# Kernel optimization log

Hardware: AMD Instinct MI355X
Metric: run time of the kernel (lower is better)

## Reference

```python
import jax, jax.numpy as jnp
import numpy as np

# ---- model hyperparameters (match init_kwargs) ----
THRESHOLD = 1.0
DECAY = 0.9
RESET = 0.0
BATCH = 256
INPUT_DIM = 1024
HIDDEN_DIM = 2048
OUTPUT_DIM = 10
NUM_LAYERS = 2
SIM_STEPS = 100
SPIKE_PROB = 0.2  # density of input spike bins


def setup_inputs() -> dict:
    key = jax.random.key(0)
    k1, k2, k3, k4 = jax.random.split(key, 4)
    # binary spike bins: [B, input_dim, T]
    input_bins = (jax.random.uniform(k1, (BATCH, INPUT_DIM, SIM_STEPS)) < SPIKE_PROB).astype(jnp.float32)
    W_ih = jax.random.normal(k2, (INPUT_DIM, HIDDEN_DIM), dtype=jnp.float32) * 0.1
    W_hh = jax.random.normal(k3, (NUM_LAYERS - 1, HIDDEN_DIM, HIDDEN_DIM), dtype=jnp.float32) * 0.1
    W_ho = jax.random.normal(k4, (HIDDEN_DIM, OUTPUT_DIM), dtype=jnp.float32) * 0.1
    return {"input_bins": input_bins, "W_ih": W_ih, "W_hh": W_hh, "W_ho": W_ho}


def _lif_step(v, current):
    """One leaky-integrate-and-fire update. v, current: [B, N]."""
    v = v * DECAY + current
    spiked = v >= THRESHOLD
    spikes = jnp.where(spiked, 1.0, 0.0).astype(v.dtype)
    v = jnp.where(spiked, RESET, v)
    return v, spikes


def reference(input_bins, W_ih, W_hh, W_ho):
    B = input_bins.shape[0]
    T = input_bins.shape[2]
    x = jnp.transpose(input_bins, (2, 0, 1))  # [T, B, input_dim]
    v_hidden = tuple(jnp.zeros((B, W_ih.shape[1]), input_bins.dtype) for _ in range(NUM_LAYERS))
    v_out = jnp.zeros((B, W_ho.shape[1]), input_bins.dtype)

    def step(carry, inp_t):
        vs, vo = carry
        vs = list(vs)
        vs[0], s = _lif_step(vs[0], inp_t @ W_ih)
        for i in range(NUM_LAYERS - 1):
            vs[i + 1], s = _lif_step(vs[i + 1], s @ W_hh[i])
        # modulator signal is 0 here -> output_input * (1 + 0*0.1) = output_input
        vo, s_out = _lif_step(vo, s @ W_ho)
        return (tuple(vs), vo), s_out

    _, out_spikes = jax.lax.scan(step, (v_hidden, v_out), x)  # [T, B, output_dim]
    output_rates = out_spikes.sum(axis=0) / T  # [B, output_dim]
    return output_rates
```

## Files before the change

### kernel.cpp

```cpp
#include <hip/hip_runtime.h>
#include <hip/hip_bf16.h>


#define B 256
#define IN_DIM 1024
#define HID 2048
#define OUT_DIM 10
#define T_STEPS 100
#define NCH 4
#define RT (T_STEPS * B)

typedef unsigned long long ull;
typedef int v4i __attribute__((ext_vector_type(4)));

template<int K>
__global__ __launch_bounds__(256) void cvt_w_i8(
    const float* __restrict__ W, signed char* __restrict__ Bq)
{
    constexpr int WPR = K / 64;
    size_t id = (size_t)blockIdx.x * 256 + threadIdx.x;
    if (id >= (size_t)(K / 4) * HID) return;
    int n  = (int)(id % HID);
    int kg = (int)(id / HID);
    int k0 = kg * 4;
    signed char dig[4][4];
#pragma unroll
    for (int i = 0; i < 4; ++i) {
        double w = (double)W[(size_t)(k0 + i) * HID + n];
        long long V = __double2ll_rn(w * 2147483648.0);
#pragma unroll
        for (int c = 0; c < 3; ++c) {
            int r = (int)(signed char)(V & 0xFF);
            dig[c][i] = (signed char)r;
            V = (V - r) >> 8;
        }
        dig[3][i] = (signed char)V;
    }
    int wb = k0 >> 6, lk = (k0 >> 4) & 3, jj = k0 & 15;
    int nb32 = n >> 5, ct = (n >> 4) & 1, li = n & 15;
    int lane = lk * 16 + li;
    size_t base = ((size_t)nb32 * WPR + wb) * 8192 + (size_t)lane * 16 + jj;
#pragma unroll
    for (int c = 0; c < 4; ++c) {
        int pc = (c < 3) ? (c * 2 + ct) : (6 + ct);
        unsigned pk = (unsigned)(unsigned char)dig[c][0]
                    | ((unsigned)(unsigned char)dig[c][1] << 8)
                    | ((unsigned)(unsigned char)dig[c][2] << 16)
                    | ((unsigned)(unsigned char)dig[c][3] << 24);
        *reinterpret_cast<unsigned*>(Bq + base + (size_t)pc * 1024) = pk;
    }
}

__global__ __launch_bounds__(256) void cvt_who(
    const float* __restrict__ who, double* __restrict__ Who64)
{
    int i = blockIdx.x * 256 + threadIdx.x;
    if (i < HID * OUT_DIM) Who64[i] = (double)who[i];
}

__global__ __launch_bounds__(256) void bitpack_input(
    const float* __restrict__ inp, ull* __restrict__ XbitsT)
{
    int g = blockIdx.x * 4 + (threadIdx.x >> 6);
    int lane = threadIdx.x & 63;
    int b = g >> 4;
    int ig = g & 15;
    int i = ig * 64 + lane;
    const float4* p = (const float4*)(inp + ((size_t)b * IN_DIM + i) * T_STEPS);
    ull* dst = XbitsT + (size_t)ig * RT + b;
#pragma unroll 1
    for (int t4 = 0; t4 < T_STEPS / 4; ++t4) {
        float4 v = p[t4];
        ull m0 = __ballot(v.x > 0.5f);
        ull m1 = __ballot(v.y > 0.5f);
        ull m2 = __ballot(v.z > 0.5f);
        ull m3 = __ballot(v.w > 0.5f);
        if (lane == 0) {
            dst[(size_t)(t4 * 4 + 0) * B] = m0;
            dst[(size_t)(t4 * 4 + 1) * B] = m1;
            dst[(size_t)(t4 * 4 + 2) * B] = m2;
            dst[(size_t)(t4 * 4 + 3) * B] = m3;
        }
    }
}

template<int K>
__global__ __launch_bounds__(256, 3) void gemm_i8(
    const ull* __restrict__ bitsT, int row_base,
    const signed char* __restrict__ Bq, float* __restrict__ C)
{
    constexpr int WPR = K / 64;
    constexpr int NP  = WPR / 2;
    __shared__ __align__(16) signed char blds[6][8192];

    const int tid = threadIdx.x;
    const int lane = tid & 63;
    const int wv = __builtin_amdgcn_readfirstlane(tid >> 6);
    const int row0 = blockIdx.x * 128;
    const int c0 = blockIdx.y * 32;
    const int li = lane & 15;
    const int lk = lane >> 4;
    const int sh = lk * 16;
    const int r0l = wv * 32;

    const signed char* __restrict__ bsrc = Bq + (size_t)blockIdx.y * WPR * 8192;
    const ull* __restrict__ m0p = bitsT + (row_base + row0 + r0l + li);
    const ull* __restrict__ m1p = m0p + 16;

    auto stage_b = [&](int w, int slot) {
        const signed char* src = bsrc + (size_t)w * 8192 + lane * 16;
        signed char* db = &blds[0][0] + slot * 8192;
        __builtin_amdgcn_global_load_lds(
            (const __attribute__((address_space(1))) unsigned int*)(src + wv * 1024),
            (__attribute__((address_space(3))) unsigned int*)(db + wv * 1024), 16, 0, 0);
        __builtin_amdgcn_global_load_lds(
            (const __attribute__((address_space(1))) unsigned int*)(src + (wv + 4) * 1024),
            (__attribute__((address_space(3))) unsigned int*)(db + (wv + 4) * 1024), 16, 0, 0);
    };

    stage_b(0, 0);
    stage_b(1, 1);
    stage_b(2, 2);
    stage_b(3, 3);
    ull r0[4], r1[4];
#pragma unroll
    for (int u = 0; u < 4; ++u) {
        r0[u] = m0p[(size_t)u * RT];
        r1[u] = m1p[(size_t)u * RT];
    }
    __syncthreads();

    v4i acc[2][2][NCH];
#pragma unroll
    for (int g = 0; g < 2; ++g)
#pragma unroll
        for (int t = 0; t < 2; ++t)
#pragma unroll
            for (int c = 0; c < NCH; ++c) acc[g][t][c] = (v4i){0, 0, 0, 0};

    int s0 = 0;
#pragma unroll 1
    for (int p2 = 0; p2 < NP; p2 += 2) {
#pragma unroll
        for (int pp = 0; pp < 2; ++pp) {
            const int w0 = (p2 + pp) * 2;
            const int u0 = w0 & 3, u1 = (w0 + 1) & 3;
            int s1 = s0 + 1; if (s1 >= 6) s1 -= 6;
            int t0 = s0 + 4; if (t0 >= 6) t0 -= 6;
            int t1 = s0 + 5; if (t1 >= 6) t1 -= 6;

            int wn0 = w0 + 4; if (wn0 >= WPR) wn0 -= WPR;
            int wn1 = w0 + 5; if (wn1 >= WPR) wn1 -= WPR;
            stage_b(wn0, t0);
            stage_b(wn1, t1);
            ull m00 = r0[u0], m01 = r1[u0];
            ull m10 = r0[u1], m11 = r1[u1];
            r0[u0] = m0p[(size_t)wn0 * RT];
            r1[u0] = m1p[(size_t)wn0 * RT];
            r0[u1] = m0p[(size_t)wn1 * RT];
            r1[u1] = m1p[(size_t)wn1 * RT];

            {
                unsigned sa = (unsigned)(m00 >> sh) & 0xFFFFu;
                unsigned sb = (unsigned)(m01 >> sh) & 0xFFFFu;
                v4i a0, a1;
#pragma unroll
                for (int d = 0; d < 4; ++d) {
                    a0[d] = (int)((((sa >> (4 * d)) & 0xFu) * 0x00204081u) & 0x01010101u);
                    a1[d] = (int)((((sb >> (4 * d)) & 0xFu) * 0x00204081u) & 0x01010101u);
                }
                const signed char* bb = &blds[0][0] + s0 * 8192 + lane * 16;
                __builtin_amdgcn_s_setprio(1);
#pragma unroll
                for (int c = 0; c < NCH; ++c) {
#pragma unroll
                    for (int t = 0; t < 2; ++t) {
                        v4i b = *(const v4i*)(bb + (c * 2 + t) * 1024);
                        acc[0][t][c] = __builtin_amdgcn_mfma_i32_16x16x64_i8(a0, b, acc[0][t][c], 0, 0, 0);
                        acc[1][t][c] = __builtin_amdgcn_mfma_i32_16x16x64_i8(a1, b, acc[1][t][c], 0, 0, 0);
                    }
                }
                __builtin_amdgcn_s_setprio(0);
            }
            {
                unsigned sa = (unsigned)(m10 >> sh) & 0xFFFFu;
                unsigned sb = (unsigned)(m11 >> sh) & 0xFFFFu;
                v4i a0, a1;
#pragma unroll
                for (int d = 0; d < 4; ++d) {
                    a0[d] = (int)((((sa >> (4 * d)) & 0xFu) * 0x00204081u) & 0x01010101u);
                    a1[d] = (int)((((sb >> (4 * d)) & 0xFu) * 0x00204081u) & 0x01010101u);
                }
                const signed char* bb = &blds[0][0] + s1 * 8192 + lane * 16;
                __builtin_amdgcn_s_setprio(1);
#pragma unroll
                for (int c = 0; c < NCH; ++c) {
#pragma unroll
                    for (int t = 0; t < 2; ++t) {
                        v4i b = *(const v4i*)(bb + (c * 2 + t) * 1024);
                        acc[0][t][c] = __builtin_amdgcn_mfma_i32_16x16x64_i8(a0, b, acc[0][t][c], 0, 0, 0);
                        acc[1][t][c] = __builtin_amdgcn_mfma_i32_16x16x64_i8(a1, b, acc[1][t][c], 0, 0, 0);
                    }
                }
                __builtin_amdgcn_s_setprio(0);
            }

            __asm__ __volatile__("s_waitcnt vmcnt(8)\n\ts_barrier" ::: "memory");
            s0 += 2; if (s0 >= 6) s0 -= 6;
        }
    }

#pragma unroll
    for (int g = 0; g < 2; ++g) {
#pragma unroll
        for (int t = 0; t < 2; ++t) {
#pragma unroll
            for (int r = 0; r < 4; ++r) {
                long long V = (long long)acc[g][t][3][r];
                V = (V << 8) + (long long)acc[g][t][2][r];
                V = (V << 8) + (long long)acc[g][t][1][r];
                V = (V << 8) + (long long)acc[g][t][0][r];
                C[(size_t)(row0 + r0l + g * 16 + lk * 4 + r) * HID + c0 + t * 16 + li] =
                    (float)((double)V * 0x1p-31);
            }
        }
    }
}

__global__ __launch_bounds__(256) void gemm_out(
    const ull* __restrict__ bitsT, int row_base,
    const double* __restrict__ W, double* __restrict__ C3)
{
    __shared__ double part[3][64][OUT_DIM];
    const int lane = threadIdx.x & 63;
    const int sl = threadIdx.x >> 6;
    const int row = blockIdx.x * 64 + lane;

    double acc[OUT_DIM];
#pragma unroll
    for (int j = 0; j < OUT_DIM; ++j) acc[j] = 0.0;

    for (int w = sl * 8; w < sl * 8 + 8; ++w) {
        ull m = bitsT[(size_t)w * RT + row_base + row];
        const double* __restrict__ wk = W + (size_t)(w * 64) * OUT_DIM;
#pragma unroll 4
        for (int kk = 0; kk < 64; ++kk) {
            double bd = (double)(unsigned int)(m & 1ull);
            m >>= 1;
#pragma unroll
            for (int j = 0; j < OUT_DIM; ++j)
                acc[j] = fma(bd, wk[j], acc[j]);
            wk += OUT_DIM;
        }
    }
    if (sl) {
#pragma unroll
        for (int j = 0; j < OUT_DIM; ++j) part[sl - 1][lane][j] = acc[j];
    }
    __syncthreads();
    if (sl == 0) {
        double* __restrict__ crow = C3 + (size_t)row * OUT_DIM;
#pragma unroll
        for (int j = 0; j < OUT_DIM; ++j)
            crow[j] = acc[j] + part[0][lane][j] + part[1][lane][j] + part[2][lane][j];
    }
}

__global__ __launch_bounds__(256) void lif_scan(
    const float* __restrict__ C, double* __restrict__ vstate,
    ull* __restrict__ SbitsT, int row_base, int Tl, int first)
{
    int g = blockIdx.x * 4 + (threadIdx.x >> 6);
    int lane = threadIdx.x & 63;
    int b = g >> 5;
    int ng = g & 31;
    int n = ng * 64 + lane;
    const float* __restrict__ Cp = C + (size_t)b * HID + n;
    ull* __restrict__ Sp = SbitsT + (size_t)ng * RT + row_base + b;
    double v = first ? 0.0 : vstate[(size_t)b * HID + n];
    int tl = 0;
    for (; tl + 4 <= Tl; tl += 4) {
        float c0 = Cp[(size_t)(tl + 0) * (B * HID)];
        float c1 = Cp[(size_t)(tl + 1) * (B * HID)];
        float c2 = Cp[(size_t)(tl + 2) * (B * HID)];
        float c3 = Cp[(size_t)(tl + 3) * (B * HID)];
#pragma unroll
        for (int i = 0; i < 4; ++i) {
            float cc = (i == 0) ? c0 : (i == 1) ? c1 : (i == 2) ? c2 : c3;
            v = v * 0.9 + (double)cc;
            bool s = (v >= 1.0);
            if (s) v = 0.0;
            ull mask = __ballot(s);
            if (lane == 0) Sp[(size_t)(tl + i) * B] = mask;
        }
    }
    for (; tl < Tl; ++tl) {
        double c = (double)Cp[(size_t)tl * (B * HID)];
        v = v * 0.9 + c;
        bool s = (v >= 1.0);
        if (s) v = 0.0;
        ull mask = __ballot(s);
        if (lane == 0) Sp[(size_t)tl * B] = mask;
    }
    vstate[(size_t)b * HID + n] = v;
}

__global__ __launch_bounds__(256) void lif_out(
    const double* __restrict__ C3, double* __restrict__ vstate,
    int* __restrict__ cnt_state, float* __restrict__ out, int Tl, int first)
{
    int tid = blockIdx.x * 256 + threadIdx.x;
    if (tid >= B * OUT_DIM) return;
    int b = tid / OUT_DIM, o = tid % OUT_DIM;
    const double* __restrict__ Cp = C3 + (size_t)b * OUT_DIM + o;
    double v = first ? 0.0 : vstate[tid];
    int cnt = first ? 0 : cnt_state[tid];
    int tl = 0;
    for (; tl + 4 <= Tl; tl += 4) {
        double c0 = Cp[(size_t)(tl + 0) * (B * OUT_DIM)];
        double c1 = Cp[(size_t)(tl + 1) * (B * OUT_DIM)];
        double c2 = Cp[(size_t)(tl + 2) * (B * OUT_DIM)];
        double c3 = Cp[(size_t)(tl + 3) * (B * OUT_DIM)];
#pragma unroll
        for (int i = 0; i < 4; ++i) {
            double cc = (i == 0) ? c0 : (i == 1) ? c1 : (i == 2) ? c2 : c3;
            v = v * 0.9 + cc;
            if (v >= 1.0) { cnt++; v = 0.0; }
        }
    }
    for (; tl < Tl; ++tl) {
        double c = Cp[(size_t)tl * (B * OUT_DIM)];
        v = v * 0.9 + c;
        if (v >= 1.0) { cnt++; v = 0.0; }
    }
    vstate[tid] = v;
    cnt_state[tid] = cnt;
    out[tid] = (float)((double)cnt / (double)T_STEPS);
}

extern "C" void kernel_launch(void* const* d_in, const int* in_sizes, int n_in,
                              void* d_out, int out_size, void* d_ws, size_t ws_size,
                              hipStream_t stream) {
    const float* inp = (const float*)d_in[0];
    const float* wih = (const float*)d_in[1];
    const float* whh = (const float*)d_in[2];
    const float* who = (const float*)d_in[3];
    float* out = (float*)d_out;

    unsigned char* p = (unsigned char*)d_ws;
    auto alloc = [&](size_t sz) -> void* {
        void* r = (void*)p;
        p += (sz + 255) & ~(size_t)255;
        return r;
    };
    signed char* Bq1 = (signed char*)alloc((size_t)NCH * HID * IN_DIM + 4096);
    signed char* Bq2 = (signed char*)alloc((size_t)NCH * HID * HID + 4096);
    double* Who64 = (double*)alloc((size_t)HID * OUT_DIM * 8);
    ull* XbitsT = (ull*)alloc((size_t)16 * RT * 8);
    ull* S1T    = (ull*)alloc((size_t)32 * RT * 8);
    ull* S2T    = (ull*)alloc((size_t)32 * RT * 8);
    double* v1 = (double*)alloc((size_t)B * HID * 8);
    double* v2 = (double*)alloc((size_t)B * HID * 8);
    double* vo = (double*)alloc((size_t)B * OUT_DIM * 8);
    int* cnts  = (int*)alloc((size_t)B * OUT_DIM * 4);

    size_t used = (size_t)(p - (unsigned char*)d_ws);
    size_t remain = (ws_size > used) ? (ws_size - used) : 0;
    size_t per_t = (size_t)B * HID * 4 + (size_t)B * OUT_DIM * 8 + 1024;
    int CH = (int)(remain / per_t);
    if (CH > T_STEPS) CH = T_STEPS;
    if (CH < 1) CH = 1;
    double* C3 = (double*)alloc((size_t)CH * B * OUT_DIM * 8);
    float* C   = (float*)alloc((size_t)CH * B * HID * 4);

    cvt_w_i8<IN_DIM><<<((IN_DIM / 4) * HID + 255) / 256, 256, 0, stream>>>(wih, Bq1);
    cvt_w_i8<HID><<<((HID / 4) * HID + 255) / 256, 256, 0, stream>>>(whh, Bq2);
    cvt_who<<<(HID * OUT_DIM + 255) / 256, 256, 0, stream>>>(who, Who64);
    bitpack_input<<<(B * (IN_DIM / 64)) / 4, 256, 0, stream>>>(inp, XbitsT);

    for (int t0 = 0; t0 < T_STEPS; t0 += CH) {
        int L = T_STEPS - t0;
        if (L > CH) L = CH;
        int rows = L * B;
        int first = (t0 == 0) ? 1 : 0;

        gemm_i8<IN_DIM><<<dim3(rows / 128, HID / 32), 256, 0, stream>>>(
            XbitsT, t0 * B, Bq1, C);
        lif_scan<<<(B * (HID / 64)) / 4, 256, 0, stream>>>(
            C, v1, S1T, t0 * B, L, first);

        gemm_i8<HID><<<dim3(rows / 128, HID / 32), 256, 0, stream>>>(
            S1T, t0 * B, Bq2, C);
        lif_scan<<<(B * (HID / 64)) / 4, 256, 0, stream>>>(
            C, v2, S2T, t0 * B, L, first);

        gemm_out<<<rows / 64, 256, 0, stream>>>(S2T, t0 * B, Who64, C3);
        lif_out<<<(B * OUT_DIM + 255) / 256, 256, 0, stream>>>(
            C3, vo, cnts, out, L, first);
    }
}
```

Baseline: 999.0 us.

## Double the gemm_i8 row tile to 256 rows per block for B reuse

Each wave now computes 64 rows (four 16-row groups) instead of 32, so a block covers 256 rows. Every B fragment read from LDS feeds four MFMAs instead of two, which halves B staging traffic per output and the grid size. The cost is twice the accumulator registers, with occupancy lowered from 3 to 2 blocks per CU, and more outstanding spike-mask loads, so the wait count is raised to 12. The weight packing index change is a cosmetic equivalence, since for c=3 the old and new pc are the same.

```diff
diff --git a/kernel.cpp b/kernel.cpp
--- a/kernel.cpp
+++ b/kernel.cpp
@@ -42,7 +42,7 @@
     size_t base = ((size_t)nb32 * WPR + wb) * 8192 + (size_t)lane * 16 + jj;
 #pragma unroll
     for (int c = 0; c < 4; ++c) {
-        int pc = (c < 3) ? (c * 2 + ct) : (6 + ct);
+        int pc = c * 2 + ct;
         unsigned pk = (unsigned)(unsigned char)dig[c][0]
                     | ((unsigned)(unsigned char)dig[c][1] << 8)
                     | ((unsigned)(unsigned char)dig[c][2] << 16)
@@ -85,7 +85,7 @@
 }
 
 template<int K>
-__global__ __launch_bounds__(256, 3) void gemm_i8(
+__global__ __launch_bounds__(256, 2) void gemm_i8(
     const ull* __restrict__ bitsT, int row_base,
     const signed char* __restrict__ Bq, float* __restrict__ C)
 {
@@ -96,16 +96,15 @@
     const int tid = threadIdx.x;
     const int lane = tid & 63;
     const int wv = __builtin_amdgcn_readfirstlane(tid >> 6);
-    const int row0 = blockIdx.x * 128;
+    const int row0 = blockIdx.x * 256;
     const int c0 = blockIdx.y * 32;
     const int li = lane & 15;
     const int lk = lane >> 4;
     const int sh = lk * 16;
-    const int r0l = wv * 32;
+    const int r0l = wv * 64;
 
     const signed char* __restrict__ bsrc = Bq + (size_t)blockIdx.y * WPR * 8192;
-    const ull* __restrict__ m0p = bitsT + (row_base + row0 + r0l + li);
-    const ull* __restrict__ m1p = m0p + 16;
+    const ull* __restrict__ mp = bitsT + (row_base + row0 + r0l + li);
 
     auto stage_b = [&](int w, int slot) {
         const signed char* src = bsrc + (size_t)w * 8192 + lane * 16;
@@ -122,17 +121,17 @@
     stage_b(1, 1);
     stage_b(2, 2);
     stage_b(3, 3);
-    ull r0[4], r1[4];
-#pragma unroll
-    for (int u = 0; u < 4; ++u) {
-        r0[u] = m0p[(size_t)u * RT];
-        r1[u] = m1p[(size_t)u * RT];
-    }
+    ull r[4][4];
+#pragma unroll
+    for (int u = 0; u < 4; ++u)
+#pragma unroll
+        for (int g = 0; g < 4; ++g)
+            r[u][g] = mp[(size_t)u * RT + g * 16];
     __syncthreads();
 
-    v4i acc[2][2][NCH];
-#pragma unroll
-    for (int g = 0; g < 2; ++g)
+    v4i acc[4][2][NCH];
+#pragma unroll
+    for (int g = 0; g < 4; ++g)
 #pragma unroll
         for (int t = 0; t < 2; ++t)
 #pragma unroll
@@ -146,28 +145,29 @@
             const int w0 = (p2 + pp) * 2;
             const int u0 = w0 & 3, u1 = (w0 + 1) & 3;
             int s1 = s0 + 1; if (s1 >= 6) s1 -= 6;
-            int t0 = s0 + 4; if (t0 >= 6) t0 -= 6;
-            int t1 = s0 + 5; if (t1 >= 6) t1 -= 6;
+            int t0s = s0 + 4; if (t0s >= 6) t0s -= 6;
+            int t1s = s0 + 5; if (t1s >= 6) t1s -= 6;
 
             int wn0 = w0 + 4; if (wn0 >= WPR) wn0 -= WPR;
             int wn1 = w0 + 5; if (wn1 >= WPR) wn1 -= WPR;
-            stage_b(wn0, t0);
-            stage_b(wn1, t1);
-            ull m00 = r0[u0], m01 = r1[u0];
-            ull m10 = r0[u1], m11 = r1[u1];
-            r0[u0] = m0p[(size_t)wn0 * RT];
-            r1[u0] = m1p[(size_t)wn0 * RT];
-            r0[u1] = m0p[(size_t)wn1 * RT];
-            r1[u1] = m1p[(size_t)wn1 * RT];
+            stage_b(wn0, t0s);
+            stage_b(wn1, t1s);
+            ull m0[4], m1[4];
+#pragma unroll
+            for (int g = 0; g < 4; ++g) { m0[g] = r[u0][g]; m1[g] = r[u1][g]; }
+#pragma unroll
+            for (int g = 0; g < 4; ++g) r[u0][g] = mp[(size_t)wn0 * RT + g * 16];
+#pragma unroll
+            for (int g = 0; g < 4; ++g) r[u1][g] = mp[(size_t)wn1 * RT + g * 16];
 
             {
-                unsigned sa = (unsigned)(m00 >> sh) & 0xFFFFu;
-                unsigned sb = (unsigned)(m01 >> sh) & 0xFFFFu;
-                v4i a0, a1;
-#pragma unroll
-                for (int d = 0; d < 4; ++d) {
-                    a0[d] = (int)((((sa >> (4 * d)) & 0xFu) * 0x00204081u) & 0x01010101u);
-                    a1[d] = (int)((((sb >> (4 * d)) & 0xFu) * 0x00204081u) & 0x01010101u);
+                v4i a[4];
+#pragma unroll
+                for (int g = 0; g < 4; ++g) {
+                    unsigned s = (unsigned)(m0[g] >> sh) & 0xFFFFu;
+#pragma unroll
+                    for (int d = 0; d < 4; ++d)
+                        a[g][d] = (int)((((s >> (4 * d)) & 0xFu) * 0x00204081u) & 0x01010101u);
                 }
                 const signed char* bb = &blds[0][0] + s0 * 8192 + lane * 16;
                 __builtin_amdgcn_s_setprio(1);
@@ -176,20 +176,21 @@
 #pragma unroll
                     for (int t = 0; t < 2; ++t) {
                         v4i b = *(const v4i*)(bb + (c * 2 + t) * 1024);
-                        acc[0][t][c] = __builtin_amdgcn_mfma_i32_16x16x64_i8(a0, b, acc[0][t][c], 0, 0, 0);
-                        acc[1][t][c] = __builtin_amdgcn_mfma_i32_16x16x64_i8(a1, b, acc[1][t][c], 0, 0, 0);
+#pragma unroll
+                        for (int g = 0; g < 4; ++g)
+                            acc[g][t][c] = __builtin_amdgcn_mfma_i32_16x16x64_i8(a[g], b, acc[g][t][c], 0, 0, 0);
                     }
                 }
                 __builtin_amdgcn_s_setprio(0);
             }
             {
-                unsigned sa = (unsigned)(m10 >> sh) & 0xFFFFu;
-                unsigned sb = (unsigned)(m11 >> sh) & 0xFFFFu;
-                v4i a0, a1;
-#pragma unroll
-                for (int d = 0; d < 4; ++d) {
-                    a0[d] = (int)((((sa >> (4 * d)) & 0xFu) * 0x00204081u) & 0x01010101u);
-                    a1[d] = (int)((((sb >> (4 * d)) & 0xFu) * 0x00204081u) & 0x01010101u);
+                v4i a[4];
+#pragma unroll
+                for (int g = 0; g < 4; ++g) {
+                    unsigned s = (unsigned)(m1[g] >> sh) & 0xFFFFu;
+#pragma unroll
+                    for (int d = 0; d < 4; ++d)
+                        a[g][d] = (int)((((s >> (4 * d)) & 0xFu) * 0x00204081u) & 0x01010101u);
                 }
                 const signed char* bb = &blds[0][0] + s1 * 8192 + lane * 16;
                 __builtin_amdgcn_s_setprio(1);
@@ -198,29 +199,30 @@
 #pragma unroll
                     for (int t = 0; t < 2; ++t) {
                         v4i b = *(const v4i*)(bb + (c * 2 + t) * 1024);
-                        acc[0][t][c] = __builtin_amdgcn_mfma_i32_16x16x64_i8(a0, b, acc[0][t][c], 0, 0, 0);
-                        acc[1][t][c] = __builtin_amdgcn_mfma_i32_16x16x64_i8(a1, b, acc[1][t][c], 0, 0, 0);
+#pragma unroll
+                        for (int g = 0; g < 4; ++g)
+                            acc[g][t][c] = __builtin_amdgcn_mfma_i32_16x16x64_i8(a[g], b, acc[g][t][c], 0, 0, 0);
                     }
                 }
                 __builtin_amdgcn_s_setprio(0);
             }
 
-            __asm__ __volatile__("s_waitcnt vmcnt(8)\n\ts_barrier" ::: "memory");
+            __asm__ __volatile__("s_waitcnt vmcnt(12)\n\ts_barrier" ::: "memory");
             s0 += 2; if (s0 >= 6) s0 -= 6;
         }
     }
 
 #pragma unroll
-    for (int g = 0; g < 2; ++g) {
+    for (int g = 0; g < 4; ++g) {
 #pragma unroll
         for (int t = 0; t < 2; ++t) {
 #pragma unroll
-            for (int r = 0; r < 4; ++r) {
-                long long V = (long long)acc[g][t][3][r];
-                V = (V << 8) + (long long)acc[g][t][2][r];
-                V = (V << 8) + (long long)acc[g][t][1][r];
-                V = (V << 8) + (long long)acc[g][t][0][r];
-                C[(size_t)(row0 + r0l + g * 16 + lk * 4 + r) * HID + c0 + t * 16 + li] =
+            for (int rr = 0; rr < 4; ++rr) {
+                long long V = (long long)acc[g][t][3][rr];
+                V = (V << 8) + (long long)acc[g][t][2][rr];
+                V = (V << 8) + (long long)acc[g][t][1][rr];
+                V = (V << 8) + (long long)acc[g][t][0][rr];
+                C[(size_t)(row0 + r0l + g * 16 + lk * 4 + rr) * HID + c0 + t * 16 + li] =
                     (float)((double)V * 0x1p-31);
             }
         }
@@ -384,12 +386,12 @@
         int rows = L * B;
         int first = (t0 == 0) ? 1 : 0;
 
-        gemm_i8<IN_DIM><<<dim3(rows / 128, HID / 32), 256, 0, stream>>>(
+        gemm_i8<IN_DIM><<<dim3(rows / 256, HID / 32), 256, 0, stream>>>(
             XbitsT, t0 * B, Bq1, C);
         lif_scan<<<(B * (HID / 64)) / 4, 256, 0, stream>>>(
             C, v1, S1T, t0 * B, L, first);
 
-        gemm_i8<HID><<<dim3(rows / 128, HID / 32), 256, 0, stream>>>(
+        gemm_i8<HID><<<dim3(rows / 256, HID / 32), 256, 0, stream>>>(
             S1T, t0 * B, Bq2, C);
         lif_scan<<<(B * (HID / 64)) / 4, 256, 0, stream>>>(
             C, v2, S2T, t0 * B, L, first);
```

Result: slower. 1.021 ms (+2.2%).

## Software-pipeline spike-mask expansion into MFMA loop with scheduling barriers

Applied to the files above, without the earlier changes.

Expands the A-operand spike bit masks for the next k-step while the current step's int8 MFMAs run, using double-buffered fragment registers and sched_group_barrier to interleave MFMA, LDS reads and VALU work. The loop-end wait is relaxed from vmcnt(8) to vmcnt(12), so more global loads stay outstanding. The weight digit layout index is also simplified to c*2+ct. This is meant to hide the VALU expansion latency behind matrix work, at the cost of more registers and a more fragile memory-wait ordering.

```diff
diff --git a/kernel.cpp b/kernel.cpp
--- a/kernel.cpp
+++ b/kernel.cpp
@@ -42,7 +42,7 @@
     size_t base = ((size_t)nb32 * WPR + wb) * 8192 + (size_t)lane * 16 + jj;
 #pragma unroll
     for (int c = 0; c < 4; ++c) {
-        int pc = (c < 3) ? (c * 2 + ct) : (6 + ct);
+        int pc = c * 2 + ct;
         unsigned pk = (unsigned)(unsigned char)dig[c][0]
                     | ((unsigned)(unsigned char)dig[c][1] << 8)
                     | ((unsigned)(unsigned char)dig[c][2] << 16)
@@ -128,15 +128,47 @@
         r0[u] = m0p[(size_t)u * RT];
         r1[u] = m1p[(size_t)u * RT];
     }
+
+    v4i acc[2][2][NCH];
+#pragma unroll
+    for (int g = 0; g < 2; ++g)
+#pragma unroll
+        for (int t = 0; t < 2; ++t)
+#pragma unroll
+            for (int c = 0; c < NCH; ++c) acc[g][t][c] = (v4i){0, 0, 0, 0};
+
+    v4i f[2][2][2];
+    auto expand4 = [&](v4i& dst, ull m) {
+        unsigned x = (unsigned)(m >> sh) & 0xFFFFu;
+#pragma unroll
+        for (int c = 0; c < 4; ++c)
+            dst[c] = (int)((((x >> (4 * c)) & 0xFu) * 0x00204081u) & 0x01010101u);
+    };
+    expand4(f[0][0][0], r0[0]);
+    expand4(f[0][0][1], r1[0]);
+    expand4(f[0][1][0], r0[1]);
+    expand4(f[0][1][1], r1[1]);
     __syncthreads();
 
-    v4i acc[2][2][NCH];
-#pragma unroll
-    for (int g = 0; g < 2; ++g)
-#pragma unroll
-        for (int t = 0; t < 2; ++t)
-#pragma unroll
-            for (int c = 0; c < NCH; ++c) acc[g][t][c] = (v4i){0, 0, 0, 0};
+    auto mfma_step = [&](const signed char* bb, const v4i& a0, const v4i& a1,
+                         v4i& n0, v4i& n1, unsigned xn0, unsigned xn1) {
+        __builtin_amdgcn_s_setprio(1);
+#pragma unroll
+        for (int c = 0; c < NCH; ++c) {
+            v4i b0 = *(const v4i*)(bb + (c * 2 + 0) * 1024);
+            v4i b1 = *(const v4i*)(bb + (c * 2 + 1) * 1024);
+            acc[0][0][c] = __builtin_amdgcn_mfma_i32_16x16x64_i8(a0, b0, acc[0][0][c], 0, 0, 0);
+            acc[1][0][c] = __builtin_amdgcn_mfma_i32_16x16x64_i8(a1, b0, acc[1][0][c], 0, 0, 0);
+            acc[0][1][c] = __builtin_amdgcn_mfma_i32_16x16x64_i8(a0, b1, acc[0][1][c], 0, 0, 0);
+            acc[1][1][c] = __builtin_amdgcn_mfma_i32_16x16x64_i8(a1, b1, acc[1][1][c], 0, 0, 0);
+            n0[c] = (int)((((xn0 >> (4 * c)) & 0xFu) * 0x00204081u) & 0x01010101u);
+            n1[c] = (int)((((xn1 >> (4 * c)) & 0xFu) * 0x00204081u) & 0x01010101u);
+            __builtin_amdgcn_sched_group_barrier(0x100, 2, 0);
+            __builtin_amdgcn_sched_group_barrier(0x008, 4, 0);
+            __builtin_amdgcn_sched_group_barrier(0x002, 10, 0);
+        }
+        __builtin_amdgcn_s_setprio(0);
+    };
 
     int s0 = 0;
 #pragma unroll 1
@@ -144,68 +176,37 @@
 #pragma unroll
         for (int pp = 0; pp < 2; ++pp) {
             const int w0 = (p2 + pp) * 2;
-            const int u0 = w0 & 3, u1 = (w0 + 1) & 3;
+            const int u0 = (2 * pp) & 3;
+            const int u1 = u0 + 1;
             int s1 = s0 + 1; if (s1 >= 6) s1 -= 6;
-            int t0 = s0 + 4; if (t0 >= 6) t0 -= 6;
-            int t1 = s0 + 5; if (t1 >= 6) t1 -= 6;
+            int t0s = s0 + 4; if (t0s >= 6) t0s -= 6;
+            int t1s = s0 + 5; if (t1s >= 6) t1s -= 6;
 
             int wn0 = w0 + 4; if (wn0 >= WPR) wn0 -= WPR;
             int wn1 = w0 + 5; if (wn1 >= WPR) wn1 -= WPR;
-            stage_b(wn0, t0);
-            stage_b(wn1, t1);
-            ull m00 = r0[u0], m01 = r1[u0];
-            ull m10 = r0[u1], m11 = r1[u1];
+            stage_b(wn0, t0s);
+            stage_b(wn1, t1s);
+
+            ull nA0 = r0[u0 ^ 2], nA1 = r1[u0 ^ 2];
+            ull nB0 = r0[u1 ^ 2], nB1 = r1[u1 ^ 2];
+            unsigned xA0 = (unsigned)(nA0 >> sh) & 0xFFFFu;
+            unsigned xA1 = (unsigned)(nA1 >> sh) & 0xFFFFu;
+            unsigned xB0 = (unsigned)(nB0 >> sh) & 0xFFFFu;
+            unsigned xB1 = (unsigned)(nB1 >> sh) & 0xFFFFu;
+
             r0[u0] = m0p[(size_t)wn0 * RT];
             r1[u0] = m1p[(size_t)wn0 * RT];
             r0[u1] = m0p[(size_t)wn1 * RT];
             r1[u1] = m1p[(size_t)wn1 * RT];
 
-            {
-                unsigned sa = (unsigned)(m00 >> sh) & 0xFFFFu;
-                unsigned sb = (unsigned)(m01 >> sh) & 0xFFFFu;
-                v4i a0, a1;
-#pragma unroll
-                for (int d = 0; d < 4; ++d) {
-                    a0[d] = (int)((((sa >> (4 * d)) & 0xFu) * 0x00204081u) & 0x01010101u);
-                    a1[d] = (int)((((sb >> (4 * d)) & 0xFu) * 0x00204081u) & 0x01010101u);
-                }
-                const signed char* bb = &blds[0][0] + s0 * 8192 + lane * 16;
-                __builtin_amdgcn_s_setprio(1);
-#pragma unroll
-                for (int c = 0; c < NCH; ++c) {
-#pragma unroll
-                    for (int t = 0; t < 2; ++t) {
-                        v4i b = *(const v4i*)(bb + (c * 2 + t) * 1024);
-                        acc[0][t][c] = __builtin_amdgcn_mfma_i32_16x16x64_i8(a0, b, acc[0][t][c], 0, 0, 0);
-                        acc[1][t][c] = __builtin_amdgcn_mfma_i32_16x16x64_i8(a1, b, acc[1][t][c], 0, 0, 0);
-                    }
-                }
-                __builtin_amdgcn_s_setprio(0);
-            }
-            {
-                unsigned sa = (unsigned)(m10 >> sh) & 0xFFFFu;
-                unsigned sb = (unsigned)(m11 >> sh) & 0xFFFFu;
-                v4i a0, a1;
-#pragma unroll
-                for (int d = 0; d < 4; ++d) {
-                    a0[d] = (int)((((sa >> (4 * d)) & 0xFu) * 0x00204081u) & 0x01010101u);
-                    a1[d] = (int)((((sb >> (4 * d)) & 0xFu) * 0x00204081u) & 0x01010101u);
-                }
-                const signed char* bb = &blds[0][0] + s1 * 8192 + lane * 16;
-                __builtin_amdgcn_s_setprio(1);
-#pragma unroll
-                for (int c = 0; c < NCH; ++c) {
-#pragma unroll
-                    for (int t = 0; t < 2; ++t) {
-                        v4i b = *(const v4i*)(bb + (c * 2 + t) * 1024);
-                        acc[0][t][c] = __builtin_amdgcn_mfma_i32_16x16x64_i8(a0, b, acc[0][t][c], 0, 0, 0);
-                        acc[1][t][c] = __builtin_amdgcn_mfma_i32_16x16x64_i8(a1, b, acc[1][t][c], 0, 0, 0);
-                    }
-                }
-                __builtin_amdgcn_s_setprio(0);
-            }
-
-            __asm__ __volatile__("s_waitcnt vmcnt(8)\n\ts_barrier" ::: "memory");
+            const signed char* bbA = &blds[0][0] + s0 * 8192 + lane * 16;
+            const signed char* bbB = &blds[0][0] + s1 * 8192 + lane * 16;
+            mfma_step(bbA, f[pp][0][0], f[pp][0][1],
+                      f[pp ^ 1][0][0], f[pp ^ 1][0][1], xA0, xA1);
+            mfma_step(bbB, f[pp][1][0], f[pp][1][1],
+                      f[pp ^ 1][1][0], f[pp ^ 1][1][1], xB0, xB1);
+
+            __asm__ __volatile__("s_waitcnt vmcnt(12)\n\ts_barrier" ::: "memory");
             s0 += 2; if (s0 >= 6) s0 -= 6;
         }
     }
```

Result: slower. 1.052 ms (+5.3%).
